# Optimization experiments

Hardware: AMD Instinct MI355X
Metric: run time of the kernel (lower is better)

## Reference

```python
import jax, jax.numpy as jnp
import numpy as np

B, D, OUT, K = 2048, 256, 256, 16


def setup_inputs() -> dict:
    key = jax.random.key(0)
    k1, k2, k3, k4 = jax.random.split(key, 4)
    x = jax.random.normal(k1, (B, D), dtype=jnp.float32)
    values = jax.random.uniform(k2, (OUT, D, K), dtype=jnp.float32, minval=-0.05, maxval=0.05)
    skip_w = jax.random.normal(k3, (OUT, D), dtype=jnp.float32) * (1.0 / np.sqrt(D).astype(np.float32))
    skip_b = jax.random.normal(k4, (OUT,), dtype=jnp.float32) * 0.01
    return {"x": x, "values": values, "skip_w": skip_w, "skip_b": skip_b}


def reference(x, values, skip_w, skip_b):
    # x: (B, D); values: (OUT, D, K); skip_w: (OUT, D); skip_b: (OUT,)
    num_knots = values.shape[-1]
    grid = jnp.linspace(-1.0, 1.0, num_knots)  # (K,)
    xc = jnp.clip(x, -1.0, 1.0)
    # torch.bucketize(x, grid) with right=False == searchsorted side='left'
    right = jnp.searchsorted(grid, xc, side='left')
    left = jnp.clip(right - 1, 0, num_knots - 2)  # (B, D)
    right = left + 1
    g0 = grid[left]
    g1 = grid[right]
    w = (xc - g0) / (g1 - g0 + 1e-12)  # (B, D)
    # Gather spline values per (sample, input-dim) knot bucket.
    vt = jnp.transpose(values, (1, 2, 0))  # (D, K, OUT)
    dim_idx = jnp.arange(xc.shape[1])[None, :]  # (1, D)
    v_left = vt[dim_idx, left]    # (B, D, OUT)
    v_right = vt[dim_idx, right]  # (B, D, OUT)
    # Linear interpolation + sum over input dims.
    y = jnp.sum((1.0 - w)[..., None] * v_left + w[..., None] * v_right, axis=1)  # (B, OUT)
    # Skip connection on the clamped input (torch reassigns x = clamp(x) first).
    return y + xc @ skip_w.T + skip_b
```

## Files before the change

kernel.cpp:

```cpp
#include <hip/hip_runtime.h>
#include <hip/hip_bf16.h>


namespace {
constexpr int Bsz  = 2048;
constexpr int Din  = 256;
constexpr int Dout = 256;
constexpr int Kn   = 16;
constexpr int KKNOT = Din * Kn;
constexpr int Ksp   = KKNOT + Din;
constexpr int KB    = Ksp / 32;
constexpr int KBK   = KKNOT / 32;
constexpr float INV_H = 7.5f;
constexpr float Hgrid = 2.0f / 15.0f;

constexpr int NSPLIT = 17;
constexpr int SPS    = 8;
constexpr int MT     = Bsz / 64;
}

typedef __attribute__((ext_vector_type(8))) short shortx8;
typedef __attribute__((ext_vector_type(4))) float floatx4;

__device__ __forceinline__ unsigned int f2bf(float f) {
  __hip_bfloat16 h = __float2bfloat16(f);
  return (unsigned int)*reinterpret_cast<unsigned short*>(&h);
}
__device__ __forceinline__ float clamp1(float v) {
  return fminf(1.f, fmaxf(-1.f, v));
}

union FragCvt { uint4 u; shortx8 s; };

__global__ __launch_bounds__(256) void kan_prep(
    const float* __restrict__ values, const float* __restrict__ skip_w,
    unsigned short* __restrict__ Wf) {
  const int tid = blockIdx.x * 256 + threadIdx.x;
  const int q  = tid & 3;
  const int n  = (tid >> 2) & 15;
  const int og = (tid >> 6) & 15;
  const int kb = tid >> 10;
  const int o  = og * 16 + n;
  const int k0 = kb * 32 + q * 8;
  const float* src = (kb < KBK)
      ? values + (size_t)o * KKNOT + k0
      : skip_w + (size_t)o * Din + (k0 - KKNOT);
  const float4 v0 = *(const float4*)src;
  const float4 v1 = *(const float4*)(src + 4);
  const size_t chunk = (size_t)kb * 1024 + og * 64 + q * 16 + n;
  *(uint4*)(Wf + chunk * 8) = make_uint4(
      f2bf(v0.x) | (f2bf(v0.y) << 16), f2bf(v0.z) | (f2bf(v0.w) << 16),
      f2bf(v1.x) | (f2bf(v1.y) << 16), f2bf(v1.z) | (f2bf(v1.w) << 16));
}

__global__ __launch_bounds__(256) void kan_gemm(
    const float* __restrict__ x, const unsigned short* __restrict__ Wf,
    float* __restrict__ part) {
  __shared__ float sx[16 * 64];

  const int tid  = threadIdx.x;
  const int wave = tid >> 6, lane = tid & 63;
  const int ks   = blockIdx.x % NSPLIT;
  const int mi   = blockIdx.x / NSPLIT;
  const int m0   = mi * 64;
  const int ni   = wave;
  const int og0  = ni * 4;
  const int kb0  = (ks < 16) ? ks * SPS : KBK;

  const int lrow = lane & 15, lq = lane >> 4;
  const int dsel  = lq >> 1;
  const float hbase = (float)((lq & 1) * 8);

  const uint4* B = (const uint4*)Wf;

  floatx4 acc[4][4] = {};
  uint4 bb[2][4];

  if (ks < 16) {
    {
      const int row = tid >> 2, dq = tid & 3;
      const float4 v = *(const float4*)(x + (size_t)(m0 + row) * Din + ks * 16 + 4 * dq);
      sx[(4 * dq + 0) * 64 + row] = v.x;
      sx[(4 * dq + 1) * 64 + row] = v.y;
      sx[(4 * dq + 2) * 64 + row] = v.z;
      sx[(4 * dq + 3) * 64 + row] = v.w;
    }
    __syncthreads();

    #pragma unroll
    for (int j = 0; j < 4; ++j)
      bb[0][j] = B[(size_t)kb0 * 1024 + (og0 + j) * 64 + lane];

    for (int s = 0; s < SPS; ++s) {
      const int cur = s & 1, nxt = cur ^ 1;
      if (s + 1 < SPS) {
        #pragma unroll
        for (int j = 0; j < 4; ++j)
          bb[nxt][j] = B[(size_t)(kb0 + s + 1) * 1024 + (og0 + j) * 64 + lane];
      }
      const int dloc = 2 * s + dsel;
      shortx8 af[4];
      #pragma unroll
      for (int i = 0; i < 4; ++i) {
        const float xv = sx[dloc * 64 + 16 * i + lrow];
        const float t = (clamp1(xv) + 1.f) * INV_H;
        unsigned int uu[4];
        #pragma unroll
        for (int p = 0; p < 4; ++p) {
          const float e0 = fmaxf(0.f, 1.f - fabsf(t - (hbase + (float)(2 * p))));
          const float e1 = fmaxf(0.f, 1.f - fabsf(t - (hbase + (float)(2 * p + 1))));
          uu[p] = f2bf(e0) | (f2bf(e1) << 16);
        }
        FragCvt c; c.u = make_uint4(uu[0], uu[1], uu[2], uu[3]);
        af[i] = c.s;
      }
      #pragma unroll
      for (int j = 0; j < 4; ++j) {
        FragCvt bc; bc.u = bb[cur][j];
        #pragma unroll
        for (int i = 0; i < 4; ++i)
          acc[i][j] = __builtin_amdgcn_mfma_f32_16x16x32_bf16(af[i], bc.s, acc[i][j], 0, 0, 0);
      }
    }
  } else {
    #pragma unroll
    for (int j = 0; j < 4; ++j)
      bb[0][j] = B[(size_t)kb0 * 1024 + (og0 + j) * 64 + lane];

    for (int s = 0; s < SPS; ++s) {
      const int kb = kb0 + s;
      const int cur = s & 1, nxt = cur ^ 1;
      if (s + 1 < SPS) {
        #pragma unroll
        for (int j = 0; j < 4; ++j)
          bb[nxt][j] = B[(size_t)(kb + 1) * 1024 + (og0 + j) * 64 + lane];
      }
      const int xoff = (kb - KBK) * 32 + lq * 8;
      shortx8 af[4];
      #pragma unroll
      for (int i = 0; i < 4; ++i) {
        const float* xp = x + (size_t)(m0 + 16 * i + lrow) * Din + xoff;
        const float4 v0 = *(const float4*)xp;
        const float4 v1 = *(const float4*)(xp + 4);
        FragCvt c;
        c.u = make_uint4(
            f2bf(clamp1(v0.x)) | (f2bf(clamp1(v0.y)) << 16),
            f2bf(clamp1(v0.z)) | (f2bf(clamp1(v0.w)) << 16),
            f2bf(clamp1(v1.x)) | (f2bf(clamp1(v1.y)) << 16),
            f2bf(clamp1(v1.z)) | (f2bf(clamp1(v1.w)) << 16));
        af[i] = c.s;
      }
      #pragma unroll
      for (int j = 0; j < 4; ++j) {
        FragCvt bc; bc.u = bb[cur][j];
        #pragma unroll
        for (int i = 0; i < 4; ++i)
          acc[i][j] = __builtin_amdgcn_mfma_f32_16x16x32_bf16(af[i], bc.s, acc[i][j], 0, 0, 0);
      }
    }
  }

  float* P = part + (size_t)ks * Bsz * Dout;
  #pragma unroll
  for (int i = 0; i < 4; ++i) {
    const int grow = m0 + 16 * i + lq * 4;
    #pragma unroll
    for (int j = 0; j < 4; ++j) {
      const int gcol = og0 * 16 + 16 * j + lrow;
      #pragma unroll
      for (int r = 0; r < 4; ++r)
        P[(size_t)(grow + r) * Dout + gcol] = acc[i][j][r];
    }
  }
}

__global__ __launch_bounds__(256) void kan_reduce(
    const float* __restrict__ part, const float* __restrict__ skip_b,
    float* __restrict__ out) {
  const int i = blockIdx.x * 256 + threadIdx.x;
  const int base = i * 4;
  const int o = base & (Dout - 1);
  float4 a = *(const float4*)(skip_b + o);
  #pragma unroll
  for (int s = 0; s < NSPLIT; ++s) {
    const float4 p = *(const float4*)(part + (size_t)s * Bsz * Dout + base);
    a.x += p.x; a.y += p.y; a.z += p.z; a.w += p.w;
  }
  *(float4*)(out + base) = a;
}

__device__ __forceinline__ void knot_interp(float xraw, float& xv, float& w, int& l) {
  xv = fminf(1.0f, fmaxf(-1.0f, xraw));
  float t = (xv + 1.0f) * INV_H;
  l = (int)ceilf(t) - 1;
  l = l < 0 ? 0 : (l > Kn - 2 ? Kn - 2 : l);
  float g0 = -1.0f + Hgrid * (float)l;
  w = (xv - g0) * INV_H;
}

__global__ __launch_bounds__(256) void prep_transpose(
    const float* __restrict__ values, const float* __restrict__ skip_w,
    float* __restrict__ vt, float* __restrict__ swt) {
  int idx = blockIdx.x * blockDim.x + threadIdx.x;
  if (idx < Din * Kn * Dout) {
    int k = idx & (Kn - 1);
    int d = (idx >> 4) & (Din - 1);
    int o = idx >> 12;
    vt[(d * Kn + k) * Dout + o] = values[idx];
  }
  if (idx < Dout * Din) {
    int d = idx & (Din - 1);
    int o = idx >> 8;
    swt[d * Dout + o] = skip_w[idx];
  }
}

__global__ __launch_bounds__(256) void kan_main(
    const float* __restrict__ x, const float* __restrict__ vt,
    const float* __restrict__ swt, const float* __restrict__ skip_b,
    float* __restrict__ out) {
  __shared__ float s_w[4][Din];
  __shared__ float s_x[4][Din];
  __shared__ int   s_l[4][Din];
  const int tid = threadIdx.x;
  const int b0  = blockIdx.x * 4;
  for (int i = tid; i < 4 * Din; i += 256) {
    int bb = i >> 8;
    int d  = i & (Din - 1);
    float xv, w; int l;
    knot_interp(x[(b0 + bb) * Din + d], xv, w, l);
    s_w[bb][d] = w; s_x[bb][d] = xv; s_l[bb][d] = l;
  }
  __syncthreads();
  const int g = tid >> 6, lane = tid & 63;
  const int o = lane << 2, b = b0 + g;
  float4 acc = make_float4(0.f, 0.f, 0.f, 0.f);
  for (int d = 0; d < Din; ++d) {
    const float w = s_w[g][d], xv = s_x[g][d];
    const int l = s_l[g][d];
    const float* base = vt + (d * Kn + l) * Dout + o;
    const float4 vl = *(const float4*)(base);
    const float4 vr = *(const float4*)(base + Dout);
    const float4 sw = *(const float4*)(swt + d * Dout + o);
    acc.x = fmaf(xv, sw.x, fmaf(w, vr.x - vl.x, acc.x + vl.x));
    acc.y = fmaf(xv, sw.y, fmaf(w, vr.y - vl.y, acc.y + vl.y));
    acc.z = fmaf(xv, sw.z, fmaf(w, vr.z - vl.z, acc.z + vl.z));
    acc.w = fmaf(xv, sw.w, fmaf(w, vr.w - vl.w, acc.w + vl.w));
  }
  const float4 bias = *(const float4*)(skip_b + o);
  acc.x += bias.x; acc.y += bias.y; acc.z += bias.z; acc.w += bias.w;
  *(float4*)(out + (size_t)b * Dout + o) = acc;
}

extern "C" void kernel_launch(void* const* d_in, const int* in_sizes, int n_in,
                              void* d_out, int out_size, void* d_ws, size_t ws_size,
                              hipStream_t stream) {
  (void)in_sizes; (void)n_in; (void)out_size;
  const float* x      = (const float*)d_in[0];
  const float* values = (const float*)d_in[1];
  const float* skip_w = (const float*)d_in[2];
  const float* skip_b = (const float*)d_in[3];
  float* out = (float*)d_out;

  const size_t wf_bytes   = (size_t)Dout * Ksp * sizeof(unsigned short);
  const size_t part_bytes = (size_t)NSPLIT * Bsz * Dout * sizeof(float);
  const size_t need_gemm  = wf_bytes + part_bytes;
  const size_t need_fb    = (size_t)(Din * Kn * Dout + Din * Dout) * sizeof(float);

  if (ws_size >= need_gemm) {
    unsigned short* Wf = (unsigned short*)d_ws;
    float* part = (float*)((char*)d_ws + wf_bytes);
    kan_prep<<<(KB * 1024) / 256, 256, 0, stream>>>(values, skip_w, Wf);
    kan_gemm<<<MT * NSPLIT, 256, 0, stream>>>(x, Wf, part);
    kan_reduce<<<Bsz * Dout / 4 / 256, 256, 0, stream>>>(part, skip_b, out);
  } else if (ws_size >= need_fb) {
    float* vt  = (float*)d_ws;
    float* swt = vt + Din * Kn * Dout;
    prep_transpose<<<(Din * Kn * Dout + 255) / 256, 256, 0, stream>>>(values, skip_w, vt, swt);
    kan_main<<<Bsz / 4, 256, 0, stream>>>(x, vt, swt, skip_b, out);
  }
}
```

Baseline: 90.43 us.

## Share A-fragment generation through LDS and store partials in MFMA-native layout

Before, every wave built the full 64x32 bf16 A fragment for its own MFMAs, so the hat-basis math was repeated four times per block. Now each thread computes one 8-element segment, writes it to a double-buffered LDS tile, syncs, and every wave reads its fragments from there. Partial sums are written as contiguous floatx4 in accumulator order, and the reduce kernel remaps them to output coordinates and adds the bias. Bf16 conversion becomes a cheap round-half-up bit trick. This adds a __syncthreads per k-step and scattered scalar output stores in the reduce, and the rounding differs slightly from round-to-nearest-even.

```diff
diff --git a/kernel.cpp b/kernel.cpp
--- a/kernel.cpp
+++ b/kernel.cpp
@@ -17,6 +17,8 @@
 constexpr int NSPLIT = 17;
 constexpr int SPS    = 8;
 constexpr int MT     = Bsz / 64;
+constexpr int TILE_F = 64 * 64;
+constexpr int PELEM  = Bsz * Dout;
 }
 
 typedef __attribute__((ext_vector_type(8))) short shortx8;
@@ -29,8 +31,12 @@
 __device__ __forceinline__ float clamp1(float v) {
   return fminf(1.f, fmaxf(-1.f, v));
 }
-
-union FragCvt { uint4 u; shortx8 s; };
+__device__ __forceinline__ unsigned int packbf(unsigned int e0, unsigned int e1) {
+  return (e1 & 0xffff0000u) | (e0 >> 16);
+}
+__device__ __forceinline__ unsigned int rnd(float f) {
+  return __float_as_uint(f) + 0x8000u;
+}
 
 __global__ __launch_bounds__(256) void kan_prep(
     const float* __restrict__ values, const float* __restrict__ skip_w,
@@ -57,19 +63,20 @@
     const float* __restrict__ x, const unsigned short* __restrict__ Wf,
     float* __restrict__ part) {
   __shared__ float sx[16 * 64];
+  __shared__ __align__(16) unsigned short aLds[2][64 * 32];
 
   const int tid  = threadIdx.x;
   const int wave = tid >> 6, lane = tid & 63;
   const int ks   = blockIdx.x % NSPLIT;
   const int mi   = blockIdx.x / NSPLIT;
   const int m0   = mi * 64;
-  const int ni   = wave;
-  const int og0  = ni * 4;
+  const int og0  = wave * 4;
   const int kb0  = (ks < 16) ? ks * SPS : KBK;
 
   const int lrow = lane & 15, lq = lane >> 4;
-  const int dsel  = lq >> 1;
-  const float hbase = (float)((lq & 1) * 8);
+
+  const int brow_k = tid & 63, bseg_k = tid >> 6;
+  const int brow_s = tid >> 2, bseg_s = tid & 3;
 
   const uint4* B = (const uint4*)Wf;
 
@@ -77,116 +84,98 @@
   uint4 bb[2][4];
 
   if (ks < 16) {
-    {
-      const int row = tid >> 2, dq = tid & 3;
-      const float4 v = *(const float4*)(x + (size_t)(m0 + row) * Din + ks * 16 + 4 * dq);
-      sx[(4 * dq + 0) * 64 + row] = v.x;
-      sx[(4 * dq + 1) * 64 + row] = v.y;
-      sx[(4 * dq + 2) * 64 + row] = v.z;
-      sx[(4 * dq + 3) * 64 + row] = v.w;
+    const int row = tid >> 2, dq = tid & 3;
+    const float4 v = *(const float4*)(x + (size_t)(m0 + row) * Din + ks * 16 + 4 * dq);
+    sx[(4 * dq + 0) * 64 + row] = v.x;
+    sx[(4 * dq + 1) * 64 + row] = v.y;
+    sx[(4 * dq + 2) * 64 + row] = v.z;
+    sx[(4 * dq + 3) * 64 + row] = v.w;
+    __syncthreads();
+  }
+
+  #pragma unroll
+  for (int j = 0; j < 4; ++j)
+    bb[0][j] = B[(size_t)kb0 * 1024 + (og0 + j) * 64 + lane];
+
+  for (int s = 0; s < SPS; ++s) {
+    const int cur = s & 1;
+    if (s + 1 < SPS) {
+      #pragma unroll
+      for (int j = 0; j < 4; ++j)
+        bb[cur ^ 1][j] = B[(size_t)(kb0 + s + 1) * 1024 + (og0 + j) * 64 + lane];
+    }
+
+    if (ks < 16) {
+      const int dloc = 2 * s + (bseg_k >> 1);
+      const float xv = sx[dloc * 64 + brow_k];
+      const float t  = (clamp1(xv) + 1.f) * INV_H;
+      const float h0 = (float)((bseg_k & 1) * 8);
+      unsigned int e[8];
+      #pragma unroll
+      for (int h = 0; h < 8; ++h)
+        e[h] = rnd(fmaxf(0.f, 1.f - fabsf(t - (h0 + (float)h))));
+      *(uint4*)((char*)&aLds[cur][0] + brow_k * 64 + bseg_k * 16) =
+          make_uint4(packbf(e[0], e[1]), packbf(e[2], e[3]),
+                     packbf(e[4], e[5]), packbf(e[6], e[7]));
+    } else {
+      const float* xp = x + (size_t)(m0 + brow_s) * Din + (kb0 + s - KBK) * 32 + bseg_s * 8;
+      const float4 v0 = *(const float4*)xp;
+      const float4 v1 = *(const float4*)(xp + 4);
+      unsigned int e[8];
+      e[0] = rnd(clamp1(v0.x)); e[1] = rnd(clamp1(v0.y));
+      e[2] = rnd(clamp1(v0.z)); e[3] = rnd(clamp1(v0.w));
+      e[4] = rnd(clamp1(v1.x)); e[5] = rnd(clamp1(v1.y));
+      e[6] = rnd(clamp1(v1.z)); e[7] = rnd(clamp1(v1.w));
+      *(uint4*)((char*)&aLds[cur][0] + brow_s * 64 + bseg_s * 16) =
+          make_uint4(packbf(e[0], e[1]), packbf(e[2], e[3]),
+                     packbf(e[4], e[5]), packbf(e[6], e[7]));
     }
     __syncthreads();
 
+    shortx8 af[4];
+    #pragma unroll
+    for (int i = 0; i < 4; ++i)
+      af[i] = *(const shortx8*)((const char*)&aLds[cur][0] + (16 * i + lrow) * 64 + lq * 16);
+
+    #pragma unroll
+    for (int j = 0; j < 4; ++j) {
+      union { uint4 u; shortx8 s; } bc;
+      bc.u = bb[cur][j];
+      #pragma unroll
+      for (int i = 0; i < 4; ++i)
+        acc[i][j] = __builtin_amdgcn_mfma_f32_16x16x32_bf16(af[i], bc.s, acc[i][j], 0, 0, 0);
+    }
+  }
+
+  float* P = part + (size_t)ks * PELEM + (size_t)(mi * 4 + wave) * TILE_F;
+  #pragma unroll
+  for (int i = 0; i < 4; ++i)
     #pragma unroll
     for (int j = 0; j < 4; ++j)
-      bb[0][j] = B[(size_t)kb0 * 1024 + (og0 + j) * 64 + lane];
-
-    for (int s = 0; s < SPS; ++s) {
-      const int cur = s & 1, nxt = cur ^ 1;
-      if (s + 1 < SPS) {
-        #pragma unroll
-        for (int j = 0; j < 4; ++j)
-          bb[nxt][j] = B[(size_t)(kb0 + s + 1) * 1024 + (og0 + j) * 64 + lane];
-      }
-      const int dloc = 2 * s + dsel;
-      shortx8 af[4];
-      #pragma unroll
-      for (int i = 0; i < 4; ++i) {
-        const float xv = sx[dloc * 64 + 16 * i + lrow];
-        const float t = (clamp1(xv) + 1.f) * INV_H;
-        unsigned int uu[4];
-        #pragma unroll
-        for (int p = 0; p < 4; ++p) {
-          const float e0 = fmaxf(0.f, 1.f - fabsf(t - (hbase + (float)(2 * p))));
-          const float e1 = fmaxf(0.f, 1.f - fabsf(t - (hbase + (float)(2 * p + 1))));
-          uu[p] = f2bf(e0) | (f2bf(e1) << 16);
-        }
-        FragCvt c; c.u = make_uint4(uu[0], uu[1], uu[2], uu[3]);
-        af[i] = c.s;
-      }
-      #pragma unroll
-      for (int j = 0; j < 4; ++j) {
-        FragCvt bc; bc.u = bb[cur][j];
-        #pragma unroll
-        for (int i = 0; i < 4; ++i)
-          acc[i][j] = __builtin_amdgcn_mfma_f32_16x16x32_bf16(af[i], bc.s, acc[i][j], 0, 0, 0);
-      }
-    }
-  } else {
-    #pragma unroll
-    for (int j = 0; j < 4; ++j)
-      bb[0][j] = B[(size_t)kb0 * 1024 + (og0 + j) * 64 + lane];
-
-    for (int s = 0; s < SPS; ++s) {
-      const int kb = kb0 + s;
-      const int cur = s & 1, nxt = cur ^ 1;
-      if (s + 1 < SPS) {
-        #pragma unroll
-        for (int j = 0; j < 4; ++j)
-          bb[nxt][j] = B[(size_t)(kb + 1) * 1024 + (og0 + j) * 64 + lane];
-      }
-      const int xoff = (kb - KBK) * 32 + lq * 8;
-      shortx8 af[4];
-      #pragma unroll
-      for (int i = 0; i < 4; ++i) {
-        const float* xp = x + (size_t)(m0 + 16 * i + lrow) * Din + xoff;
-        const float4 v0 = *(const float4*)xp;
-        const float4 v1 = *(const float4*)(xp + 4);
-        FragCvt c;
-        c.u = make_uint4(
-            f2bf(clamp1(v0.x)) | (f2bf(clamp1(v0.y)) << 16),
-            f2bf(clamp1(v0.z)) | (f2bf(clamp1(v0.w)) << 16),
-            f2bf(clamp1(v1.x)) | (f2bf(clamp1(v1.y)) << 16),
-            f2bf(clamp1(v1.z)) | (f2bf(clamp1(v1.w)) << 16));
-        af[i] = c.s;
-      }
-      #pragma unroll
-      for (int j = 0; j < 4; ++j) {
-        FragCvt bc; bc.u = bb[cur][j];
-        #pragma unroll
-        for (int i = 0; i < 4; ++i)
-          acc[i][j] = __builtin_amdgcn_mfma_f32_16x16x32_bf16(af[i], bc.s, acc[i][j], 0, 0, 0);
-      }
-    }
-  }
-
-  float* P = part + (size_t)ks * Bsz * Dout;
-  #pragma unroll
-  for (int i = 0; i < 4; ++i) {
-    const int grow = m0 + 16 * i + lq * 4;
-    #pragma unroll
-    for (int j = 0; j < 4; ++j) {
-      const int gcol = og0 * 16 + 16 * j + lrow;
-      #pragma unroll
-      for (int r = 0; r < 4; ++r)
-        P[(size_t)(grow + r) * Dout + gcol] = acc[i][j][r];
-    }
-  }
+      *(floatx4*)&P[((i * 4 + j) * 64 + lane) * 4] = acc[i][j];
 }
 
 __global__ __launch_bounds__(256) void kan_reduce(
     const float* __restrict__ part, const float* __restrict__ skip_b,
     float* __restrict__ out) {
-  const int i = blockIdx.x * 256 + threadIdx.x;
-  const int base = i * 4;
-  const int o = base & (Dout - 1);
-  float4 a = *(const float4*)(skip_b + o);
+  const int tid = blockIdx.x * 256 + threadIdx.x;
+  float4 a = make_float4(0.f, 0.f, 0.f, 0.f);
   #pragma unroll
   for (int s = 0; s < NSPLIT; ++s) {
-    const float4 p = *(const float4*)(part + (size_t)s * Bsz * Dout + base);
+    const float4 p = *(const float4*)(part + (size_t)s * PELEM + (size_t)tid * 4);
     a.x += p.x; a.y += p.y; a.z += p.z; a.w += p.w;
   }
-  *(float4*)(out + base) = a;
+  const int f4   = tid & 1023, tile = tid >> 10;
+  const int ij   = f4 >> 6,   lane = f4 & 63;
+  const int i    = ij >> 2,   j    = ij & 3;
+  const int mi   = tile >> 2, ni   = tile & 3;
+  const int b0   = mi * 64 + 16 * i + (lane >> 4) * 4;
+  const int o    = ni * 64 + 16 * j + (lane & 15);
+  const float sb = skip_b[o];
+  out[(size_t)(b0 + 0) * Dout + o] = a.x + sb;
+  out[(size_t)(b0 + 1) * Dout + o] = a.y + sb;
+  out[(size_t)(b0 + 2) * Dout + o] = a.z + sb;
+  out[(size_t)(b0 + 3) * Dout + o] = a.w + sb;
 }
 
 __device__ __forceinline__ void knot_interp(float xraw, float& xv, float& w, int& l) {
@@ -263,7 +252,7 @@
   float* out = (float*)d_out;
 
   const size_t wf_bytes   = (size_t)Dout * Ksp * sizeof(unsigned short);
-  const size_t part_bytes = (size_t)NSPLIT * Bsz * Dout * sizeof(float);
+  const size_t part_bytes = (size_t)NSPLIT * PELEM * sizeof(float);
   const size_t need_gemm  = wf_bytes + part_bytes;
   const size_t need_fb    = (size_t)(Din * Kn * Dout + Din * Dout) * sizeof(float);
 
@@ -272,7 +261,7 @@
     float* part = (float*)((char*)d_ws + wf_bytes);
     kan_prep<<<(KB * 1024) / 256, 256, 0, stream>>>(values, skip_w, Wf);
     kan_gemm<<<MT * NSPLIT, 256, 0, stream>>>(x, Wf, part);
-    kan_reduce<<<Bsz * Dout / 4 / 256, 256, 0, stream>>>(part, skip_b, out);
+    kan_reduce<<<PELEM / 4 / 256, 256, 0, stream>>>(part, skip_b, out);
   } else if (ws_size >= need_fb) {
     float* vt  = (float*)d_ws;
     float* swt = vt + Din * Kn * Dout;
```

Result: faster. 81.21 us (-10.2%).
